# Kernel tuning notes

Measured on AMD Instinct MI355X. Metric: run time of the kernel, lower is better.

The kernel has to match this reference:

```python
import jax, jax.numpy as jnp
import numpy as np

B, M, D = 512, 96, 512
H = 8            # num_heads
DH = D // H      # head dim
NC = 3           # num_clusters
BETA = 5
MEM = 1024       # memory_size
EPS = 1e-8


def _l2norm(x, axis=-1):
    # torch F.cosine_similarity clamps each norm at eps=1e-8
    n = jnp.linalg.norm(x, axis=axis, keepdims=True)
    return x / jnp.maximum(n, EPS)


def _dynamic_clustering(sims):
    # sims: (B, M). Sort descending, split into NC equal groups,
    # per-group mean and (unbiased) std. (dynamic_clustering is not
    # defined in the source repo; this is the assumed implementation.)
    s = -jnp.sort(-sims, axis=1)               # descending
    g = s.reshape(B, NC, M // NC)
    means = g.mean(axis=-1)                    # (B, NC)
    stds = jnp.std(g, axis=-1, ddof=1)         # (B, NC)
    return means, stds


def setup_inputs() -> dict:
    key = jax.random.key(0)
    ks = jax.random.split(key, 6)
    vis_global = jax.random.normal(ks[0], (B, D), dtype=jnp.float32)
    text_features = jax.random.normal(ks[1], (B, M, D), dtype=jnp.float32)
    scale = 1.0 / np.sqrt(D)
    in_proj_w = jax.random.normal(ks[2], (3 * D, D), dtype=jnp.float32) * scale
    in_proj_b = jnp.zeros((3 * D,), dtype=jnp.float32)
    out_proj_w = jax.random.normal(ks[3], (D, D), dtype=jnp.float32) * scale
    out_proj_b = jnp.zeros((D,), dtype=jnp.float32)
    text_memory = jax.random.normal(ks[4], (MEM, D), dtype=jnp.float32)
    tau_p_log = jnp.log(jnp.asarray(0.1, dtype=jnp.float32))
    tau_n_log = jnp.log(jnp.asarray(0.05, dtype=jnp.float32))
    return dict(vis_global=vis_global, text_features=text_features,
                in_proj_w=in_proj_w, in_proj_b=in_proj_b,
                out_proj_w=out_proj_w, out_proj_b=out_proj_b,
                text_memory=text_memory, tau_p_log=tau_p_log, tau_n_log=tau_n_log)


def reference(vis_global, text_features, in_proj_w, in_proj_b,
              out_proj_w, out_proj_b, text_memory, tau_p_log, tau_n_log):
    # --- dynamic clustering over visual-text cosine sims ---
    sims = jnp.einsum('bd,bmd->bm', _l2norm(vis_global), _l2norm(text_features))
    means, stds = _dynamic_clustering(sims)
    cluster_scores = means / (stds + 1e-6)     # (B, NC)

    # --- MultiheadAttention: 1-token query, M-token key/value ---
    wq, wk, wv = in_proj_w[:D], in_proj_w[D:2 * D], in_proj_w[2 * D:]
    bq, bk, bv = in_proj_b[:D], in_proj_b[D:2 * D], in_proj_b[2 * D:]
    q = (vis_global @ wq.T + bq).reshape(B, H, DH)              # (B,H,DH)
    k = (text_features @ wk.T + bk).reshape(B, M, H, DH)        # (B,M,H,DH)
    v = (text_features @ wv.T + bv).reshape(B, M, H, DH)
    attn = jax.nn.softmax(jnp.einsum('bhd,bmhd->bhm', q, k) / np.sqrt(DH), axis=-1)
    ctx = jnp.einsum('bhm,bmhd->bhd', attn, v).reshape(B, D)
    corrected = ctx @ out_proj_w.T + out_proj_b                 # (B, D)

    tau_p = jnp.exp(tau_p_log)
    tau_n = jnp.exp(tau_n_log)
    pos_sim = jnp.sum(_l2norm(vis_global) * _l2norm(corrected), axis=-1)  # (B,)

    # memory-bank scatter (ptr starts at 0) + negatives, all detached
    corr_sg = jax.lax.stop_gradient(corrected)
    mem = text_memory.at[0:B].set(corr_sg)
    all_negs = jnp.concatenate([jnp.roll(corr_sg, 1, axis=0), mem], axis=0)  # (B+MEM, D)

    neg_sims = _l2norm(vis_global) @ _l2norm(all_negs).T        # (B, B+MEM)
    hard_negs, _ = jax.lax.top_k(neg_sims, BETA)                # (B, BETA)

    pos_term = jnp.exp(pos_sim / tau_p)
    neg_terms = jnp.exp(hard_negs / tau_n).sum(axis=1)
    loss = -jnp.mean(jnp.log(pos_term / (pos_term + neg_terms + 1e-8)))
    return loss, corrected, cluster_scores
```

## Files before the change

### kernel.cpp

```cpp
#include <hip/hip_runtime.h>
#include <math.h>

typedef unsigned short u16;
typedef unsigned int u32;
typedef __attribute__((ext_vector_type(8))) short short8;
typedef __attribute__((ext_vector_type(8))) _Float16 half8;
typedef __attribute__((ext_vector_type(4))) float f32x4;

#define EPS 1e-8f

__device__ inline float bf2f(u16 u) {
    union { u32 i; float f; } v; v.i = ((u32)u) << 16; return v.f;
}
__device__ inline u16 f2bf(float f) {
    union { float f; u32 u; } v; v.f = f;
    u32 r = v.u + 0x7fffu + ((v.u >> 16) & 1u);
    return (u16)(r >> 16);
}
__device__ inline u16 f2h(float f) {
    _Float16 h = (_Float16)f;
    union { _Float16 hh; u16 u; } v; v.hh = h; return v.u;
}
__device__ inline u32 pack2(float a, float b) {
    return (u32)f2bf(a) | ((u32)f2bf(b) << 16);
}
__device__ inline float wave_sum(float v) {
    for (int off = 32; off; off >>= 1) v += __shfl_xor(v, off, 64);
    return v;
}

__device__ __forceinline__ void stage64x512(const u16* __restrict__ Ag, size_t lda,
                                            u16* __restrict__ As) {
    const int t = threadIdx.x;
    const int srow = t >> 2;
    const int c0 = (t & 3) * 8;
    #pragma unroll
    for (int kk = 0; kk < 16; kk++) {
        int c = c0 + kk * 32;
        *(uint4*)&As[srow * 520 + c] = *(const uint4*)&Ag[(size_t)srow * lda + c];
    }
}
__device__ __forceinline__ void mfma_k512(const u16* __restrict__ As,
                                          const u16* __restrict__ Bs,
                                          f32x4 (&acc)[2][2]) {
    const int t = threadIdx.x, lane = t & 63, w = t >> 6;
    const int wm = (w >> 1) * 32, wn = (w & 1) * 32;
    const int l16 = lane & 15, quad = lane >> 4;
    #pragma unroll
    for (int ks = 0; ks < 16; ks++) {
        short8 af[2], bfr[2];
        #pragma unroll
        for (int i = 0; i < 2; i++)
            af[i] = *(const short8*)&As[(wm + i * 16 + l16) * 520 + ks * 32 + quad * 8];
        #pragma unroll
        for (int j = 0; j < 2; j++)
            bfr[j] = *(const short8*)&Bs[(wn + j * 16 + l16) * 520 + ks * 32 + quad * 8];
        #pragma unroll
        for (int i = 0; i < 2; i++)
            #pragma unroll
            for (int j = 0; j < 2; j++)
                acc[i][j] = __builtin_amdgcn_mfma_f32_16x16x32_bf16(af[i], bfr[j], acc[i][j], 0, 0, 0);
    }
}

__global__ __launch_bounds__(256) void prep(const float* __restrict__ vis,
                                            const float* __restrict__ ipw,
                                            const float* __restrict__ opw,
                                            const float* __restrict__ tm,
                                            float* __restrict__ vis_n,
                                            u16* __restrict__ vis_nb,
                                            u16* __restrict__ vis_b,
                                            u16* __restrict__ wqb,
                                            u16* __restrict__ wvb,
                                            u16* __restrict__ wob,
                                            u16* __restrict__ negsb,
                                            u16* __restrict__ wkT,
                                            float* __restrict__ corrSS,
                                            float* __restrict__ loss0)
{
    int bid = blockIdx.x;
    int t = threadIdx.x;
    if (bid >= 1024) {
        __shared__ __align__(16) u16 T[64 * 72];
        int idx = bid - 1024;
        int a = idx >> 3, cb = idx & 7;
        const float* wk = ipw + 262144;
        int r = t >> 2, c0 = (t & 3) * 16;
        #pragma unroll
        for (int q = 0; q < 4; q++) {
            float4 v = *(const float4*)&wk[(size_t)(a * 64 + r) * 512 + cb * 64 + c0 + q * 4];
            T[(c0 + q * 4 + 0) * 72 + r] = f2h(v.x);
            T[(c0 + q * 4 + 1) * 72 + r] = f2h(v.y);
            T[(c0 + q * 4 + 2) * 72 + r] = f2h(v.z);
            T[(c0 + q * 4 + 3) * 72 + r] = f2h(v.w);
        }
        __syncthreads();
        int j = t >> 2, ch = (t & 3) * 16;
        *(uint4*)&wkT[(size_t)(cb * 64 + j) * 512 + a * 64 + ch]     = *(const uint4*)&T[j * 72 + ch];
        *(uint4*)&wkT[(size_t)(cb * 64 + j) * 512 + a * 64 + ch + 8] = *(const uint4*)&T[j * 72 + ch + 8];
        return;
    }
    if (bid >= 896) {
        int wave = t >> 6, lane = t & 63;
        int j = 512 + (bid - 896) * 4 + wave;
        const float* row = tm + (size_t)(j - 512) * 512 + lane * 8;
        float4 x0 = *(const float4*)row;
        float4 x1 = *(const float4*)(row + 4);
        float ss = x0.x*x0.x + x0.y*x0.y + x0.z*x0.z + x0.w*x0.w
                 + x1.x*x1.x + x1.y*x1.y + x1.z*x1.z + x1.w*x1.w;
        ss = wave_sum(ss);
        float inv = 1.0f / fmaxf(sqrtf(ss), EPS);
        uint4 pk;
        pk.x = pack2(x0.x*inv, x0.y*inv); pk.y = pack2(x0.z*inv, x0.w*inv);
        pk.z = pack2(x1.x*inv, x1.y*inv); pk.w = pack2(x1.z*inv, x1.w*inv);
        *(uint4*)(negsb + (size_t)j * 512 + lane * 8) = pk;
        return;
    }
    if (bid >= 128) {
        int i = ((bid - 128) * 256 + t) * 4;
        const float* src; u16* dst; int j;
        if (i < 262144)      { j = i;          src = ipw + j;          dst = wqb + j; }
        else if (i < 524288) { j = i - 262144; src = ipw + 524288 + j; dst = wvb + j; }
        else                 { j = i - 524288; src = opw + j;          dst = wob + j; }
        float4 v = *(const float4*)src;
        uint2 pk; pk.x = pack2(v.x, v.y); pk.y = pack2(v.z, v.w);
        *(uint2*)dst = pk;
        return;
    }
    if (bid == 0) {
        if (t == 0) loss0[0] = 0.0f;
        corrSS[t] = 0.0f;
        corrSS[t + 256] = 0.0f;
    }
    int wave = t >> 6, lane = t & 63;
    int b = bid * 4 + wave;
    const float* row = vis + (size_t)b * 512 + lane * 8;
    float4 x0 = *(const float4*)row;
    float4 x1 = *(const float4*)(row + 4);
    uint4 rk;
    rk.x = pack2(x0.x, x0.y); rk.y = pack2(x0.z, x0.w);
    rk.z = pack2(x1.x, x1.y); rk.w = pack2(x1.z, x1.w);
    *(uint4*)(vis_b + (size_t)b * 512 + lane * 8) = rk;
    float ss = x0.x*x0.x + x0.y*x0.y + x0.z*x0.z + x0.w*x0.w
             + x1.x*x1.x + x1.y*x1.y + x1.z*x1.z + x1.w*x1.w;
    ss = wave_sum(ss);
    float inv = 1.0f / fmaxf(sqrtf(ss), EPS);
    float4 y0, y1;
    y0.x = x0.x*inv; y0.y = x0.y*inv; y0.z = x0.z*inv; y0.w = x0.w*inv;
    y1.x = x1.x*inv; y1.y = x1.y*inv; y1.z = x1.z*inv; y1.w = x1.w*inv;
    *(float4*)(vis_n + (size_t)b * 512 + lane * 8)     = y0;
    *(float4*)(vis_n + (size_t)b * 512 + lane * 8 + 4) = y1;
    uint4 pk;
    pk.x = pack2(y0.x, y0.y); pk.y = pack2(y0.z, y0.w);
    pk.z = pack2(y1.x, y1.y); pk.w = pack2(y1.z, y1.w);
    *(uint4*)(vis_nb + (size_t)b * 512 + lane * 8) = pk;
}

__global__ __launch_bounds__(256) void mid(const u16* __restrict__ visb,
                                           const u16* __restrict__ vis_nb,
                                           const u16* __restrict__ wqb,
                                           const float* __restrict__ ipb,
                                           const u16* __restrict__ wkT,
                                           u16* __restrict__ qkb,
                                           const u16* __restrict__ negsb,
                                           float* __restrict__ ns,
                                           const float* __restrict__ tf,
                                           const float* __restrict__ vis_n,
                                           u16* __restrict__ tfb,
                                           float* __restrict__ simsG)
{
    __shared__ __align__(16) u16 SM[3 * 64 * 72];
    const int bid = blockIdx.x;
    const int t = threadIdx.x, lane = t & 63, w = t >> 6;

    if (bid >= 128) {
        int g = (bid - 128) * 4 + w;
        #pragma unroll 2
        for (int i = 0; i < 8; i++) {
            int r = g * 8 + i;
            int b = r / 96;
            const float* row = tf + (size_t)r * 512 + lane * 8;
            float4 x0 = *(const float4*)row;
            float4 x1 = *(const float4*)(row + 4);
            const float* vn = vis_n + (size_t)b * 512 + lane * 8;
            float4 v0 = *(const float4*)vn;
            float4 v1 = *(const float4*)(vn + 4);
            float ss = x0.x*x0.x + x0.y*x0.y + x0.z*x0.z + x0.w*x0.w
                     + x1.x*x1.x + x1.y*x1.y + x1.z*x1.z + x1.w*x1.w;
            float dt = x0.x*v0.x + x0.y*v0.y + x0.z*v0.z + x0.w*v0.w
                     + x1.x*v1.x + x1.y*v1.y + x1.z*v1.z + x1.w*v1.w;
            #pragma unroll
            for (int off = 32; off; off >>= 1) {
                ss += __shfl_xor(ss, off, 64);
                dt += __shfl_xor(dt, off, 64);
            }
            uint4 pk;
            pk.x = pack2(x0.x, x0.y); pk.y = pack2(x0.z, x0.w);
            pk.z = pack2(x1.x, x1.y); pk.w = pack2(x1.z, x1.w);
            *(uint4*)(tfb + (size_t)r * 512 + lane * 8) = pk;
            if (lane == 0) simsG[r] = dt / fmaxf(sqrtf(ss), EPS);
        }
        return;
    }

    const int wm = (w >> 1) * 32, wn = (w & 1) * 32;
    const int l16 = lane & 15, quad = lane >> 4;
    const int srow = t >> 3, scol = (t & 7) * 8;

    if (bid >= 64) {
        u16* As = SM;
        u16* Bs = SM + 4608;
        int idx = bid - 64;
        int m0 = (idx & 7) * 64, n0 = (idx >> 3) * 64;
        f32x4 acc[2][2];
        for (int i = 0; i < 2; i++)
            for (int j = 0; j < 2; j++)
                for (int e = 0; e < 4; e++) acc[i][j][e] = 0.f;
        for (int ko = 0; ko < 512; ko += 64) {
            __syncthreads();
            #pragma unroll
            for (int i = 0; i < 2; i++) {
                int row = i * 32 + srow;
                *(uint4*)&As[row * 72 + scol] = *(const uint4*)&vis_nb[(size_t)(m0 + row) * 512 + ko + scol];
                *(uint4*)&Bs[row * 72 + scol] = *(const uint4*)&negsb[(size_t)(512 + n0 + row) * 512 + ko + scol];
            }
            __syncthreads();
            #pragma unroll
            for (int ks = 0; ks < 2; ks++) {
                short8 af[2], bfr[2];
                #pragma unroll
                for (int i = 0; i < 2; i++)
                    af[i] = *(const short8*)&As[(wm + i * 16 + l16) * 72 + ks * 32 + quad * 8];
                #pragma unroll
                for (int j = 0; j < 2; j++)
                    bfr[j] = *(const short8*)&Bs[(wn + j * 16 + l16) * 72 + ks * 32 + quad * 8];
                #pragma unroll
                for (int i = 0; i < 2; i++)
                    #pragma unroll
                    for (int j = 0; j < 2; j++)
                        acc[i][j] = __builtin_amdgcn_mfma_f32_16x16x32_bf16(af[i], bfr[j], acc[i][j], 0, 0, 0);
            }
        }
        #pragma unroll
        for (int i = 0; i < 2; i++)
            #pragma unroll
            for (int j = 0; j < 2; j++)
                #pragma unroll
                for (int r = 0; r < 4; r++) {
                    int row = m0 + wm + i * 16 + quad * 4 + r;
                    int col = 512 + n0 + wn + j * 16 + l16;
                    ns[(size_t)row * 1024 + col] = acc[i][j][r];
                }
        return;
    }

    u16* As = SM;
    u16* Bs = SM + 4608;
    u16* Qf = SM + 9216;
    const int m0 = (bid & 7) * 64, h = bid >> 3;

    f32x4 acc[2][2];
    for (int i = 0; i < 2; i++)
        for (int j = 0; j < 2; j++)
            for (int e = 0; e < 4; e++) acc[i][j][e] = 0.f;

    for (int ko = 0; ko < 512; ko += 64) {
        __syncthreads();
        #pragma unroll
        for (int i = 0; i < 2; i++) {
            int row = i * 32 + srow;
            *(uint4*)&As[row * 72 + scol] = *(const uint4*)&visb[(size_t)(m0 + row) * 512 + ko + scol];
            *(uint4*)&Bs[row * 72 + scol] = *(const uint4*)&wqb[(size_t)(h * 64 + row) * 512 + ko + scol];
        }
        __syncthreads();
        #pragma unroll
        for (int ks = 0; ks < 2; ks++) {
            short8 af[2], bfr[2];
            #pragma unroll
            for (int i = 0; i < 2; i++)
                af[i] = *(const short8*)&As[(wm + i * 16 + l16) * 72 + ks * 32 + quad * 8];
            #pragma unroll
            for (int j = 0; j < 2; j++)
                bfr[j] = *(const short8*)&Bs[(wn + j * 16 + l16) * 72 + ks * 32 + quad * 8];
            #pragma unroll
            for (int i = 0; i < 2; i++)
                #pragma unroll
                for (int j = 0; j < 2; j++)
                    acc[i][j] = __builtin_amdgcn_mfma_f32_16x16x32_bf16(af[i], bfr[j], acc[i][j], 0, 0, 0);
        }
    }
    #pragma unroll
    for (int i = 0; i < 2; i++)
        #pragma unroll
        for (int j = 0; j < 2; j++)
            #pragma unroll
            for (int r = 0; r < 4; r++) {
                int rl = wm + i * 16 + quad * 4 + r;
                int cl = wn + j * 16 + l16;
                Qf[rl * 72 + cl] = f2h(acc[i][j][r] + ipb[h * 64 + cl]);
            }
    for (int jt = 0; jt < 8; jt++) {
        __syncthreads();
        #pragma unroll
        for (int i = 0; i < 2; i++) {
            int row = i * 32 + srow;
            *(uint4*)&Bs[row * 72 + scol] = *(const uint4*)&wkT[(size_t)(jt * 64 + row) * 512 + h * 64 + scol];
        }
        __syncthreads();
        f32x4 a2[2][2];
        for (int i = 0; i < 2; i++)
            for (int j = 0; j < 2; j++)
                for (int e = 0; e < 4; e++) a2[i][j][e] = 0.f;
        #pragma unroll
        for (int ks = 0; ks < 2; ks++) {
            half8 af[2], bfr[2];
            #pragma unroll
            for (int i = 0; i < 2; i++)
                af[i] = *(const half8*)&Qf[(wm + i * 16 + l16) * 72 + ks * 32 + quad * 8];
            #pragma unroll
            for (int j = 0; j < 2; j++)
                bfr[j] = *(const half8*)&Bs[(wn + j * 16 + l16) * 72 + ks * 32 + quad * 8];
            #pragma unroll
            for (int i = 0; i < 2; i++)
                #pragma unroll
                for (int j = 0; j < 2; j++)
                    a2[i][j] = __builtin_amdgcn_mfma_f32_16x16x32_f16(af[i], bfr[j], a2[i][j], 0, 0, 0);
        }
        #pragma unroll
        for (int i = 0; i < 2; i++)
            #pragma unroll
            for (int j = 0; j < 2; j++)
                #pragma unroll
                for (int r = 0; r < 4; r++) {
                    int rb = m0 + wm + i * 16 + quad * 4 + r;
                    int cj = jt * 64 + wn + j * 16 + l16;
                    qkb[((size_t)rb * 8 + h) * 512 + cj] = f2bf(a2[i][j][r]);
                }
    }
}

__global__ __launch_bounds__(1024) void attn(const u16* __restrict__ tfb,
                                             const float* __restrict__ simsG,
                                             const u16* __restrict__ qkb,
                                             u16* __restrict__ u_allb,
                                             float* __restrict__ out_cs)
{
    __shared__ __align__(16) u16 Xs[96 * 520];
    __shared__ __align__(16) u16 Qs[16 * 520];
    __shared__ __align__(16) u16 Ps[16 * 104];
    __shared__ float Sc[16 * 100];
    __shared__ float sm_[96], srt[96], linv[8];

    const int b = blockIdx.x;
    const int t = threadIdx.x, w = t >> 6, lane = t & 63;
    const int l16 = lane & 15, quad = lane >> 4;

    if (t < 96) sm_[t] = simsG[b * 96 + t];
    #pragma unroll
    for (int i = 0; i < 6; i++) {
        int row = w + i * 16;
        *(uint4*)&Xs[row * 520 + lane * 8] =
            *(const uint4*)&tfb[((size_t)b * 96 + row) * 512 + lane * 8];
    }
    if (w < 8) {
        *(uint4*)&Qs[w * 520 + lane * 8] = *(const uint4*)(qkb + ((size_t)b * 8 + w) * 512 + lane * 8);
    } else {
        uint4 z; z.x = 0; z.y = 0; z.z = 0; z.w = 0;
        *(uint4*)&Qs[w * 520 + lane * 8] = z;
    }
    __syncthreads();

    if (w < 6) {
        f32x4 acc;
        for (int e = 0; e < 4; e++) acc[e] = 0.f;
        #pragma unroll
        for (int ks = 0; ks < 16; ks++) {
            short8 a = *(const short8*)&Xs[(w * 16 + l16) * 520 + ks * 32 + quad * 8];
            short8 q = *(const short8*)&Qs[l16 * 520 + ks * 32 + quad * 8];
            acc = __builtin_amdgcn_mfma_f32_16x16x32_bf16(a, q, acc, 0, 0, 0);
        }
        #pragma unroll
        for (int r = 0; r < 4; r++)
            Sc[l16 * 100 + w * 16 + quad * 4 + r] = acc[r] * 0.125f;
    }
    __syncthreads();

    if (w < 8) {
        float e0 = __expf(Sc[w * 100 + lane]);
        float e1 = (lane < 32) ? __expf(Sc[w * 100 + 64 + lane]) : 0.f;
        float l = wave_sum(e0 + e1);
        Ps[w * 104 + lane] = f2bf(e0);
        if (lane < 32) Ps[w * 104 + 64 + lane] = f2bf(e1);
        if (lane == 0) linv[w] = 1.0f / l;
    } else {
        Ps[w * 104 + lane] = 0;
        if (lane < 40) Ps[w * 104 + 64 + lane] = 0;
    }
    if (t < 96) {
        float v = sm_[t]; int r = 0;
        for (int j = 0; j < 96; j++) {
            float u = sm_[j];
            r += (u > v) || (u == v && j < t);
        }
        srt[r] = v;
    }
    __syncthreads();

    #pragma unroll
    for (int jj = 0; jj < 2; jj++) {
        int n0 = (w * 2 + jj) * 16;
        f32x4 acc;
        for (int e = 0; e < 4; e++) acc[e] = 0.f;
        #pragma unroll
        for (int ks = 0; ks < 3; ks++) {
            short8 ap = *(const short8*)&Ps[l16 * 104 + ks * 32 + quad * 8];
            short8 bx;
            #pragma unroll
            for (int j = 0; j < 8; j++)
                bx[j] = (short)Xs[(ks * 32 + quad * 8 + j) * 520 + n0 + l16];
            acc = __builtin_amdgcn_mfma_f32_16x16x32_bf16(ap, bx, acc, 0, 0, 0);
        }
        if (quad < 2) {
            #pragma unroll
            for (int r = 0; r < 4; r++) {
                int h = quad * 4 + r;
                u_allb[((size_t)b * 8 + h) * 512 + n0 + l16] = f2bf(acc[r] * linv[h]);
            }
        }
    }
    if (t < 3) {
        float mean = 0.f;
        #pragma unroll 8
        for (int i = 0; i < 32; i++) mean += srt[t * 32 + i];
        mean *= (1.0f / 32.0f);
        float var = 0.f;
        #pragma unroll 8
        for (int i = 0; i < 32; i++) { float d = srt[t * 32 + i] - mean; var += d * d; }
        var *= (1.0f / 31.0f);
        out_cs[b * 3 + t] = mean / (sqrtf(var) + 1e-6f);
    }
}

__global__ __launch_bounds__(256) void ghead(const u16* __restrict__ u_allb,
                                             const u16* __restrict__ wvb,
                                             const float* __restrict__ bv,
                                             u16* __restrict__ ctxb)
{
    __shared__ __align__(16) u16 As[64 * 520];
    __shared__ __align__(16) u16 Bs[64 * 520];
    const int bid = blockIdx.x;
    const int m0 = (bid & 7) * 64, h = bid >> 3;
    const int t = threadIdx.x, lane = t & 63, w = t >> 6;
    const int wm = (w >> 1) * 32, wn = (w & 1) * 32;
    const int l16 = lane & 15, quad = lane >> 4;

    f32x4 acc[2][2];
    for (int i = 0; i < 2; i++)
        for (int j = 0; j < 2; j++)
            for (int e = 0; e < 4; e++) acc[i][j][e] = 0.f;

    stage64x512(u_allb + (size_t)m0 * 4096 + (size_t)h * 512, 4096, As);
    stage64x512(wvb + (size_t)h * 64 * 512, 512, Bs);
    __syncthreads();
    mfma_k512(As, Bs, acc);

    for (int i = 0; i < 2; i++) {
        int row = m0 + wm + i * 16 + quad * 4;
        for (int j = 0; j < 2; j++) {
            int col = wn + j * 16 + l16;
            float bb = bv[h * 64 + col];
            for (int r = 0; r < 4; r++)
                ctxb[(size_t)(row + r) * 512 + h * 64 + col] = f2bf(acc[i][j][r] + bb);
        }
    }
}

__global__ __launch_bounds__(256) void gcorr(const u16* __restrict__ ctxb,
                                             const u16* __restrict__ wob,
                                             const float* __restrict__ bias,
                                             float* __restrict__ Cf,
                                             u16* __restrict__ corrB,
                                             float* __restrict__ corrSS)
{
    __shared__ __align__(16) u16 As[64 * 520];
    __shared__ __align__(16) u16 Bs[64 * 520];
    const int bid = blockIdx.x;
    const int m0 = (bid & 7) * 64, n0 = (bid >> 3) * 64;
    const int t = threadIdx.x, lane = t & 63, w = t >> 6;
    const int wm = (w >> 1) * 32, wn = (w & 1) * 32;
    const int l16 = lane & 15, quad = lane >> 4;

    f32x4 acc[2][2];
    for (int i = 0; i < 2; i++)
        for (int j = 0; j < 2; j++)
            for (int e = 0; e < 4; e++) acc[i][j][e] = 0.f;

    stage64x512(ctxb + (size_t)m0 * 512, 512, As);
    stage64x512(wob + (size_t)n0 * 512, 512, Bs);
    __syncthreads();
    mfma_k512(As, Bs, acc);

    #pragma unroll
    for (int i = 0; i < 2; i++) {
        #pragma unroll
        for (int r = 0; r < 4; r++) {
            int row = m0 + wm + i * 16 + quad * 4 + r;
            float s = 0.f;
            #pragma unroll
            for (int j = 0; j < 2; j++) {
                int col = n0 + wn + j * 16 + l16;
                float v = acc[i][j][r] + bias[col];
                Cf[(size_t)row * 512 + col] = v;
                corrB[(size_t)row * 512 + col] = f2bf(v);
                s += v * v;
            }
            s += __shfl_xor(s, 1, 64); s += __shfl_xor(s, 2, 64);
            s += __shfl_xor(s, 4, 64); s += __shfl_xor(s, 8, 64);
            if (l16 == 0) atomicAdd(&corrSS[row], s);
        }
    }
}

__global__ __launch_bounds__(256) void nsleft(const u16* __restrict__ vis_nb,
                                              const u16* __restrict__ negsb,
                                              float* __restrict__ ns)
{
    __shared__ __align__(16) u16 As[64 * 520];
    __shared__ __align__(16) u16 Bs[64 * 520];
    const int bid = blockIdx.x;
    const int m0 = (bid & 7) * 64, n0 = (bid >> 3) * 64;
    const int t = threadIdx.x, lane = t & 63, w = t >> 6;
    const int wm = (w >> 1) * 32, wn = (w & 1) * 32;
    const int l16 = lane & 15, quad = lane >> 4;

    f32x4 acc[2][2];
    for (int i = 0; i < 2; i++)
        for (int j = 0; j < 2; j++)
            for (int e = 0; e < 4; e++) acc[i][j][e] = 0.f;

    stage64x512(vis_nb + (size_t)m0 * 512, 512, As);
    stage64x512(negsb + (size_t)n0 * 512, 512, Bs);
    __syncthreads();
    mfma_k512(As, Bs, acc);

    for (int i = 0; i < 2; i++) {
        int row = m0 + wm + i * 16 + quad * 4;
        for (int j = 0; j < 2; j++) {
            int col = n0 + wn + j * 16 + l16;
            for (int r = 0; r < 4; r++)
                ns[(size_t)(row + r) * 1024 + col] = acc[i][j][r];
        }
    }
}

__global__ __launch_bounds__(256) void topk_loss(const float* __restrict__ ns,
                                                 const float* __restrict__ corrSS,
                                                 const float* __restrict__ tau_p_log,
                                                 const float* __restrict__ tau_n_log,
                                                 float* __restrict__ out_loss)
{
    __shared__ float invn[512];
    __shared__ float cv[20];
    __shared__ int   cjx[20];
    int b = blockIdx.x, t = threadIdx.x;
    int w = t >> 6, lane = t & 63;

    {
        float s0 = corrSS[t], s1 = corrSS[t + 256];
        invn[t]       = 1.0f / fmaxf(sqrtf(s0), EPS);
        invn[t + 256] = 1.0f / fmaxf(sqrtf(s1), EPS);
    }
    __syncthreads();

    const float4 raw = *(const float4*)(ns + (size_t)b * 1024 + t * 4);
    float lv[4] = {raw.x, raw.y, raw.z, raw.w};
    int   li[4] = {t * 4, t * 4 + 1, t * 4 + 2, t * 4 + 3};
    if (t < 128) {
        lv[0] *= invn[t * 4];     lv[1] *= invn[t * 4 + 1];
        lv[2] *= invn[t * 4 + 2]; lv[3] *= invn[t * 4 + 3];
    }
    #pragma unroll
    for (int i = 1; i < 4; i++) {
        float kv = lv[i]; int kx = li[i];
        int j = i - 1;
        #pragma unroll
        for (int k = 0; k < 3; k++) {
            if (j >= 0 && lv[j] < kv) { lv[j + 1] = lv[j]; li[j + 1] = li[j]; j--; }
        }
        lv[j + 1] = kv; li[j + 1] = kx;
    }
    int lp = 0;
    #pragma unroll
    for (int rd = 0; rd < 5; rd++) {
        float mv = (lp < 4) ? lv[lp] : -1e30f;
        int   mi = (lp < 4) ? li[lp] : 0;
        int   ml = lane;
        #pragma unroll
        for (int off = 32; off; off >>= 1) {
            float ov = __shfl_xor(mv, off, 64);
            int   oi = __shfl_xor(mi, off, 64);
            int   ol = __shfl_xor(ml, off, 64);
            if (ov > mv || (ov == mv && ol < ml)) { mv = ov; mi = oi; ml = ol; }
        }
        if (lane == ml) lp++;
        if (lane == 0) { cv[w * 5 + rd] = mv; cjx[w * 5 + rd] = mi; }
    }
    __syncthreads();
    if (w == 0) {
        float v  = (lane < 20) ? cv[lane] : -1e30f;
        int   jx = (lane < 20) ? cjx[lane] : 0;
        float tn = expf(tau_n_log[0]);
        float itn = 1.0f / tn;
        float nsum = 0.f; int coll = 0;
        #pragma unroll
        for (int rd = 0; rd < 5; rd++) {
            float mv = v; int ml = lane; int mj = jx;
            #pragma unroll
            for (int off = 32; off; off >>= 1) {
                float ov = __shfl_xor(mv, off, 64);
                int   oj = __shfl_xor(mj, off, 64);
                int   ol = __shfl_xor(ml, off, 64);
                if (ov > mv || (ov == mv && ol < ml)) { mv = ov; mj = oj; ml = ol; }
            }
            int mult = (mj < 512) ? 2 : 1;
            int take = 5 - coll;
            take = (mult < take) ? mult : take;
            if (take < 0) take = 0;
            nsum += (float)take * __expf(mv * itn);
            coll += take;
            if (lane == ml) v = -1e30f;
        }
        if (lane == 0) {
            float pos = ns[(size_t)b * 1024 + b] * invn[b];
            float tp = expf(tau_p_log[0]);
            float p = expf(pos / tp);
            float term = logf(p / (p + nsum + 1e-8f));
            atomicAdd(out_loss, -term * (1.0f / 512.0f));
        }
    }
}

extern "C" void kernel_launch(void* const* d_in, const int* in_sizes, int n_in,
                              void* d_out, int out_size, void* d_ws, size_t ws_size,
                              hipStream_t stream) {
    const float* vis = (const float*)d_in[0];
    const float* tf  = (const float*)d_in[1];
    const float* ipw = (const float*)d_in[2];
    const float* ipb = (const float*)d_in[3];
    const float* opw = (const float*)d_in[4];
    const float* opb = (const float*)d_in[5];
    const float* tm  = (const float*)d_in[6];
    const float* tpl = (const float*)d_in[7];
    const float* tnl = (const float*)d_in[8];

    float* out       = (float*)d_out;
    float* out_loss  = out;
    float* out_corr  = out + 1;
    float* out_cs    = out + 1 + 512 * 512;

    char* p = (char*)d_ws;
    auto alloc = [&](size_t bytes) { char* r = p; p += (bytes + 255) & ~(size_t)255; return r; };
    float* vis_n  = (float*)alloc(512 * 512 * 4);
    u16*   vis_nb = (u16*)  alloc(512 * 512 * 2);
    u16*   vis_b  = (u16*)  alloc(512 * 512 * 2);
    u16*   wqb    = (u16*)  alloc(512 * 512 * 2);
    u16*   wvb    = (u16*)  alloc(512 * 512 * 2);
    u16*   wob    = (u16*)  alloc(512 * 512 * 2);
    u16*   wkT    = (u16*)  alloc(512 * 512 * 2);
    u16*   qkb    = (u16*)  alloc((size_t)512 * 8 * 512 * 2);
    u16*   u_allb = (u16*)  alloc((size_t)512 * 8 * 512 * 2);
    u16*   tfb    = (u16*)  alloc((size_t)512 * 96 * 512 * 2);
    float* simsG  = (float*)alloc((size_t)512 * 96 * 4);
    u16*   ctxb   = (u16*)  alloc(512 * 512 * 2);
    u16*   negsb  = (u16*)  alloc(1024 * 512 * 2);
    float* ns     = (float*)alloc(512 * 1024 * 4);
    float* corrSS = (float*)alloc(512 * 4);

    const float* bv = ipb + 2 * 512;

    prep<<<1088, 256, 0, stream>>>(vis, ipw, opw, tm, vis_n, vis_nb, vis_b,
                                   wqb, wvb, wob, negsb, wkT, corrSS, out_loss);
    mid<<<1664, 256, 0, stream>>>(vis_b, vis_nb, wqb, ipb, wkT, qkb, negsb, ns,
                                  tf, vis_n, tfb, simsG);
    attn<<<512, 1024, 0, stream>>>(tfb, simsG, qkb, u_allb, out_cs);
    ghead<<<64, 256, 0, stream>>>(u_allb, wvb, bv, ctxb);
    gcorr<<<64, 256, 0, stream>>>(ctxb, wob, opb, out_corr, negsb, corrSS);
    nsleft<<<64, 256, 0, stream>>>(vis_nb, negsb, ns);
    topk_loss<<<512, 256, 0, stream>>>(ns, corrSS, tpl, tnl, out_loss);
}
```

Measured before the change: 232.9 us.

## Fuse tail GEMMs into one kernel with flag sync; reassociate negative sims via Wo

Replaces the ghead, gcorr and nsleft launches with a single tail kernel whose blocks wait on per-row-tile atomic flags for ctx results. The left half of the negative-similarity matrix becomes G·ctx^T plus a bias term, with G = vis_n·Wo computed earlier in mid and vb = vis_n·out_proj_b. This removes the bf16 corrected round-trip and takes nsleft off the serial dependency chain. In exchange it adds spin-wait inter-block synchronization, which assumes co-residency of producer blocks, and a different bf16 rounding path for the negative similarities.

Measured after the change: 249.0 us. 1.07x slower.

```diff
diff --git a/kernel.cpp b/kernel.cpp
--- a/kernel.cpp
+++ b/kernel.cpp
@@ -75,11 +75,32 @@
                                             u16* __restrict__ wob,
                                             u16* __restrict__ negsb,
                                             u16* __restrict__ wkT,
+                                            u16* __restrict__ woT,
                                             float* __restrict__ corrSS,
+                                            u32* __restrict__ flags,
                                             float* __restrict__ loss0)
 {
     int bid = blockIdx.x;
     int t = threadIdx.x;
+    if (bid >= 1088) {
+        __shared__ __align__(16) u16 T[64 * 72];
+        int idx = bid - 1088;
+        int a = idx >> 3, cb = idx & 7;
+        int r = t >> 2, c0 = (t & 3) * 16;
+        #pragma unroll
+        for (int q = 0; q < 4; q++) {
+            float4 v = *(const float4*)&opw[(size_t)(a * 64 + r) * 512 + cb * 64 + c0 + q * 4];
+            T[(c0 + q * 4 + 0) * 72 + r] = f2bf(v.x);
+            T[(c0 + q * 4 + 1) * 72 + r] = f2bf(v.y);
+            T[(c0 + q * 4 + 2) * 72 + r] = f2bf(v.z);
+            T[(c0 + q * 4 + 3) * 72 + r] = f2bf(v.w);
+        }
+        __syncthreads();
+        int j = t >> 2, ch = (t & 3) * 16;
+        *(uint4*)&woT[(size_t)(cb * 64 + j) * 512 + a * 64 + ch]     = *(const uint4*)&T[j * 72 + ch];
+        *(uint4*)&woT[(size_t)(cb * 64 + j) * 512 + a * 64 + ch + 8] = *(const uint4*)&T[j * 72 + ch + 8];
+        return;
+    }
     if (bid >= 1024) {
         __shared__ __align__(16) u16 T[64 * 72];
         int idx = bid - 1024;
@@ -129,6 +150,7 @@
     }
     if (bid == 0) {
         if (t == 0) loss0[0] = 0.0f;
+        if (t < 8) flags[t] = 0u;
         corrSS[t] = 0.0f;
         corrSS[t + 256] = 0.0f;
     }
@@ -164,6 +186,10 @@
                                            u16* __restrict__ qkb,
                                            const u16* __restrict__ negsb,
                                            float* __restrict__ ns,
+                                           const u16* __restrict__ woT,
+                                           u16* __restrict__ G,
+                                           const float* __restrict__ opb,
+                                           float* __restrict__ vb,
                                            const float* __restrict__ tf,
                                            const float* __restrict__ vis_n,
                                            u16* __restrict__ tfb,
@@ -173,8 +199,8 @@
     const int bid = blockIdx.x;
     const int t = threadIdx.x, lane = t & 63, w = t >> 6;
 
-    if (bid >= 128) {
-        int g = (bid - 128) * 4 + w;
+    if (bid >= 200) {
+        int g = (bid - 200) * 4 + w;
         #pragma unroll 2
         for (int i = 0; i < 8; i++) {
             int r = g * 8 + i;
@@ -202,6 +228,22 @@
         }
         return;
     }
+    if (bid >= 192) {
+        int idx = bid - 192;
+        #pragma unroll 2
+        for (int k = 0; k < 16; k++) {
+            int b = idx * 64 + w * 16 + k;
+            const float* vn = vis_n + (size_t)b * 512 + lane * 8;
+            float4 a = *(const float4*)vn, c = *(const float4*)(vn + 4);
+            const float* bo = opb + lane * 8;
+            float4 b0 = *(const float4*)bo, b1 = *(const float4*)(bo + 4);
+            float dt = a.x*b0.x + a.y*b0.y + a.z*b0.z + a.w*b0.w
+                     + c.x*b1.x + c.y*b1.y + c.z*b1.z + c.w*b1.w;
+            dt = wave_sum(dt);
+            if (lane == 0) vb[b] = dt;
+        }
+        return;
+    }
 
     const int wm = (w >> 1) * 32, wn = (w & 1) * 32;
     const int l16 = lane & 15, quad = lane >> 4;
@@ -210,8 +252,11 @@
     if (bid >= 64) {
         u16* As = SM;
         u16* Bs = SM + 4608;
-        int idx = bid - 64;
+        bool isG = (bid >= 128);
+        int idx = bid - (isG ? 128 : 64);
         int m0 = (idx & 7) * 64, n0 = (idx >> 3) * 64;
+        const u16* Bsrc = isG ? (woT + (size_t)n0 * 512)
+                              : (negsb + (size_t)(512 + n0) * 512);
         f32x4 acc[2][2];
         for (int i = 0; i < 2; i++)
             for (int j = 0; j < 2; j++)
@@ -222,7 +267,7 @@
             for (int i = 0; i < 2; i++) {
                 int row = i * 32 + srow;
                 *(uint4*)&As[row * 72 + scol] = *(const uint4*)&vis_nb[(size_t)(m0 + row) * 512 + ko + scol];
-                *(uint4*)&Bs[row * 72 + scol] = *(const uint4*)&negsb[(size_t)(512 + n0 + row) * 512 + ko + scol];
+                *(uint4*)&Bs[row * 72 + scol] = *(const uint4*)&Bsrc[(size_t)row * 512 + ko + scol];
             }
             __syncthreads();
             #pragma unroll
@@ -248,8 +293,9 @@
                 #pragma unroll
                 for (int r = 0; r < 4; r++) {
                     int row = m0 + wm + i * 16 + quad * 4 + r;
-                    int col = 512 + n0 + wn + j * 16 + l16;
-                    ns[(size_t)row * 1024 + col] = acc[i][j][r];
+                    int col = n0 + wn + j * 16 + l16;
+                    if (isG) G[(size_t)row * 512 + col] = f2bf(acc[i][j][r]);
+                    else     ns[(size_t)row * 1024 + 512 + col] = acc[i][j][r];
                 }
         return;
     }
@@ -441,15 +487,22 @@
     }
 }
 
-__global__ __launch_bounds__(256) void ghead(const u16* __restrict__ u_allb,
-                                             const u16* __restrict__ wvb,
-                                             const float* __restrict__ bv,
-                                             u16* __restrict__ ctxb)
+__global__ __launch_bounds__(256) void tail(const u16* __restrict__ u_allb,
+                                            const u16* __restrict__ wvb,
+                                            const float* __restrict__ bv,
+                                            u16* __restrict__ ctxb,
+                                            const u16* __restrict__ wob,
+                                            const float* __restrict__ bias,
+                                            float* __restrict__ Cf,
+                                            float* __restrict__ corrSS,
+                                            const u16* __restrict__ G,
+                                            const float* __restrict__ vb,
+                                            float* __restrict__ ns,
+                                            u32* __restrict__ flags)
 {
     __shared__ __align__(16) u16 As[64 * 520];
     __shared__ __align__(16) u16 Bs[64 * 520];
     const int bid = blockIdx.x;
-    const int m0 = (bid & 7) * 64, h = bid >> 3;
     const int t = threadIdx.x, lane = t & 63, w = t >> 6;
     const int wm = (w >> 1) * 32, wn = (w & 1) * 32;
     const int l16 = lane & 15, quad = lane >> 4;
@@ -459,96 +512,78 @@
         for (int j = 0; j < 2; j++)
             for (int e = 0; e < 4; e++) acc[i][j][e] = 0.f;
 
-    stage64x512(u_allb + (size_t)m0 * 4096 + (size_t)h * 512, 4096, As);
-    stage64x512(wvb + (size_t)h * 64 * 512, 512, Bs);
+    if (bid < 64) {
+        const int m0 = (bid & 7) * 64, h = bid >> 3;
+        stage64x512(u_allb + (size_t)m0 * 4096 + (size_t)h * 512, 4096, As);
+        stage64x512(wvb + (size_t)h * 64 * 512, 512, Bs);
+        __syncthreads();
+        mfma_k512(As, Bs, acc);
+        for (int i = 0; i < 2; i++) {
+            int row = m0 + wm + i * 16 + quad * 4;
+            for (int j = 0; j < 2; j++) {
+                int col = wn + j * 16 + l16;
+                float bb = bv[h * 64 + col];
+                for (int r = 0; r < 4; r++)
+                    ctxb[(size_t)(row + r) * 512 + h * 64 + col] = f2bf(acc[i][j][r] + bb);
+            }
+        }
+        __threadfence();
+        __syncthreads();
+        if (t == 0)
+            __hip_atomic_fetch_add(&flags[bid & 7], 1u, __ATOMIC_RELEASE, __HIP_MEMORY_SCOPE_AGENT);
+        return;
+    }
+
+    if (bid < 128) {
+        const int idx = bid - 64;
+        const int m0 = (idx & 7) * 64, n0 = (idx >> 3) * 64;
+        if (t == 0) {
+            while (__hip_atomic_load(&flags[idx & 7], __ATOMIC_ACQUIRE, __HIP_MEMORY_SCOPE_AGENT) < 8u)
+                __builtin_amdgcn_s_sleep(4);
+        }
+        __syncthreads();
+        stage64x512(ctxb + (size_t)m0 * 512, 512, As);
+        stage64x512(wob + (size_t)n0 * 512, 512, Bs);
+        __syncthreads();
+        mfma_k512(As, Bs, acc);
+        #pragma unroll
+        for (int i = 0; i < 2; i++) {
+            #pragma unroll
+            for (int r = 0; r < 4; r++) {
+                int row = m0 + wm + i * 16 + quad * 4 + r;
+                float s = 0.f;
+                #pragma unroll
+                for (int j = 0; j < 2; j++) {
+                    int col = n0 + wn + j * 16 + l16;
+                    float v = acc[i][j][r] + bias[col];
+                    Cf[(size_t)row * 512 + col] = v;
+                    s += v * v;
+                }
+                s += __shfl_xor(s, 1, 64); s += __shfl_xor(s, 2, 64);
+                s += __shfl_xor(s, 4, 64); s += __shfl_xor(s, 8, 64);
+                if (l16 == 0) atomicAdd(&corrSS[row], s);
+            }
+        }
+        return;
+    }
+
+    const int idx = bid - 128;
+    const int m0 = (idx & 7) * 64, n0 = (idx >> 3) * 64;
+    if (t == 0) {
+        while (__hip_atomic_load(&flags[idx >> 3], __ATOMIC_ACQUIRE, __HIP_MEMORY_SCOPE_AGENT) < 8u)
+            __builtin_amdgcn_s_sleep(4);
+    }
+    __syncthreads();
+    stage64x512(G + (size_t)m0 * 512, 512, As);
+    stage64x512(ctxb + (size_t)n0 * 512, 512, Bs);
     __syncthreads();
     mfma_k512(As, Bs, acc);
-
-    for (int i = 0; i < 2; i++) {
-        int row = m0 + wm + i * 16 + quad * 4;
-        for (int j = 0; j < 2; j++) {
-            int col = wn + j * 16 + l16;
-            float bb = bv[h * 64 + col];
-            for (int r = 0; r < 4; r++)
-                ctxb[(size_t)(row + r) * 512 + h * 64 + col] = f2bf(acc[i][j][r] + bb);
-        }
-    }
-}
-
-__global__ __launch_bounds__(256) void gcorr(const u16* __restrict__ ctxb,
-                                             const u16* __restrict__ wob,
-                                             const float* __restrict__ bias,
-                                             float* __restrict__ Cf,
-                                             u16* __restrict__ corrB,
-                                             float* __restrict__ corrSS)
-{
-    __shared__ __align__(16) u16 As[64 * 520];
-    __shared__ __align__(16) u16 Bs[64 * 520];
-    const int bid = blockIdx.x;
-    const int m0 = (bid & 7) * 64, n0 = (bid >> 3) * 64;
-    const int t = threadIdx.x, lane = t & 63, w = t >> 6;
-    const int wm = (w >> 1) * 32, wn = (w & 1) * 32;
-    const int l16 = lane & 15, quad = lane >> 4;
-
-    f32x4 acc[2][2];
-    for (int i = 0; i < 2; i++)
-        for (int j = 0; j < 2; j++)
-            for (int e = 0; e < 4; e++) acc[i][j][e] = 0.f;
-
-    stage64x512(ctxb + (size_t)m0 * 512, 512, As);
-    stage64x512(wob + (size_t)n0 * 512, 512, Bs);
-    __syncthreads();
-    mfma_k512(As, Bs, acc);
-
-    #pragma unroll
-    for (int i = 0; i < 2; i++) {
-        #pragma unroll
-        for (int r = 0; r < 4; r++) {
-            int row = m0 + wm + i * 16 + quad * 4 + r;
-            float s = 0.f;
-            #pragma unroll
-            for (int j = 0; j < 2; j++) {
-                int col = n0 + wn + j * 16 + l16;
-                float v = acc[i][j][r] + bias[col];
-                Cf[(size_t)row * 512 + col] = v;
-                corrB[(size_t)row * 512 + col] = f2bf(v);
-                s += v * v;
-            }
-            s += __shfl_xor(s, 1, 64); s += __shfl_xor(s, 2, 64);
-            s += __shfl_xor(s, 4, 64); s += __shfl_xor(s, 8, 64);
-            if (l16 == 0) atomicAdd(&corrSS[row], s);
-        }
-    }
-}
-
-__global__ __launch_bounds__(256) void nsleft(const u16* __restrict__ vis_nb,
-                                              const u16* __restrict__ negsb,
-                                              float* __restrict__ ns)
-{
-    __shared__ __align__(16) u16 As[64 * 520];
-    __shared__ __align__(16) u16 Bs[64 * 520];
-    const int bid = blockIdx.x;
-    const int m0 = (bid & 7) * 64, n0 = (bid >> 3) * 64;
-    const int t = threadIdx.x, lane = t & 63, w = t >> 6;
-    const int wm = (w >> 1) * 32, wn = (w & 1) * 32;
-    const int l16 = lane & 15, quad = lane >> 4;
-
-    f32x4 acc[2][2];
-    for (int i = 0; i < 2; i++)
-        for (int j = 0; j < 2; j++)
-            for (int e = 0; e < 4; e++) acc[i][j][e] = 0.f;
-
-    stage64x512(vis_nb + (size_t)m0 * 512, 512, As);
-    stage64x512(negsb + (size_t)n0 * 512, 512, Bs);
-    __syncthreads();
-    mfma_k512(As, Bs, acc);
-
     for (int i = 0; i < 2; i++) {
         int row = m0 + wm + i * 16 + quad * 4;
         for (int j = 0; j < 2; j++) {
             int col = n0 + wn + j * 16 + l16;
             for (int r = 0; r < 4; r++)
-                ns[(size_t)(row + r) * 1024 + col] = acc[i][j][r];
+                ns[(size_t)(row + r) * 1024 + col] = acc[i][j][r] + vb[row + r];
         }
     }
 }
@@ -667,6 +702,8 @@
     u16*   wvb    = (u16*)  alloc(512 * 512 * 2);
     u16*   wob    = (u16*)  alloc(512 * 512 * 2);
     u16*   wkT    = (u16*)  alloc(512 * 512 * 2);
+    u16*   woT    = (u16*)  alloc(512 * 512 * 2);
+    u16*   G      = (u16*)  alloc(512 * 512 * 2);
     u16*   qkb    = (u16*)  alloc((size_t)512 * 8 * 512 * 2);
     u16*   u_allb = (u16*)  alloc((size_t)512 * 8 * 512 * 2);
     u16*   tfb    = (u16*)  alloc((size_t)512 * 96 * 512 * 2);
@@ -675,16 +712,17 @@
     u16*   negsb  = (u16*)  alloc(1024 * 512 * 2);
     float* ns     = (float*)alloc(512 * 1024 * 4);
     float* corrSS = (float*)alloc(512 * 4);
+    float* vb     = (float*)alloc(512 * 4);
+    u32*   flags  = (u32*)  alloc(64 * 4);
 
     const float* bv = ipb + 2 * 512;
 
-    prep<<<1088, 256, 0, stream>>>(vis, ipw, opw, tm, vis_n, vis_nb, vis_b,
-                                   wqb, wvb, wob, negsb, wkT, corrSS, out_loss);
-    mid<<<1664, 256, 0, stream>>>(vis_b, vis_nb, wqb, ipb, wkT, qkb, negsb, ns,
-                                  tf, vis_n, tfb, simsG);
+    prep<<<1152, 256, 0, stream>>>(vis, ipw, opw, tm, vis_n, vis_nb, vis_b,
+                                   wqb, wvb, wob, negsb, wkT, woT, corrSS, flags, out_loss);
+    mid<<<1736, 256, 0, stream>>>(vis_b, vis_nb, wqb, ipb, wkT, qkb, negsb, ns,
+                                  woT, G, opb, vb, tf, vis_n, tfb, simsG);
     attn<<<512, 1024, 0, stream>>>(tfb, simsG, qkb, u_allb, out_cs);
-    ghead<<<64, 256, 0, stream>>>(u_allb, wvb, bv, ctxb);
-    gcorr<<<64, 256, 0, stream>>>(ctxb, wob, opb, out_corr, negsb, corrSS);
-    nsleft<<<64, 256, 0, stream>>>(vis_nb, negsb, ns);
+    tail<<<192, 256, 0, stream>>>(u_allb, wvb, bv, ctxb, wob, opb, out_corr, corrSS,
+                                  G, vb, ns, flags);
     topk_loss<<<512, 256, 0, stream>>>(ns, corrSS, tpl, tnl, out_loss);
 }
```
